# Kernel tuning notes

Hardware: AMD Instinct MI355X
Metric: run time of the kernel (lower is better)

Reference implementation:

```python
import jax, jax.numpy as jnp
import numpy as np

DEPTH = 6
INPUT_DIM = 512
HIDDEN = [128, 64]
OUT_DIM = 8
BATCH = 8192
NUM_LEAVES = 2 ** DEPTH            # 64
NUM_INTERNAL = 2 ** DEPTH - 1      # 63 routing Dense(1, sigmoid) nodes


def setup_inputs() -> dict:
    key = jax.random.key(0)
    ks = jax.random.split(key, 9)
    s = lambda fan_in: 1.0 / np.sqrt(fan_in)
    return {
        "x": jax.random.normal(ks[0], (BATCH, INPUT_DIM), dtype=jnp.float32),
        # routers: one Dense(input_dim -> 1) per internal node
        "router_W": jax.random.normal(ks[1], (NUM_INTERNAL, INPUT_DIM), dtype=jnp.float32) * s(INPUT_DIM),
        "router_b": jnp.zeros((NUM_INTERNAL,), dtype=jnp.float32),
        # leaf MLPs: Dense(512->128, relu) -> Dense(128->64, relu) -> Dense(64->8, linear), one per leaf
        "W1": jax.random.normal(ks[2], (NUM_LEAVES, INPUT_DIM, HIDDEN[0]), dtype=jnp.float32) * s(INPUT_DIM),
        "b1": jnp.zeros((NUM_LEAVES, HIDDEN[0]), dtype=jnp.float32),
        "W2": jax.random.normal(ks[3], (NUM_LEAVES, HIDDEN[0], HIDDEN[1]), dtype=jnp.float32) * s(HIDDEN[0]),
        "b2": jnp.zeros((NUM_LEAVES, HIDDEN[1]), dtype=jnp.float32),
        "W3": jax.random.normal(ks[4], (NUM_LEAVES, HIDDEN[1], OUT_DIM), dtype=jnp.float32) * s(HIDDEN[1]),
        "b3": jnp.zeros((NUM_LEAVES, OUT_DIM), dtype=jnp.float32),
    }


def reference(x, router_W, router_b, W1, b1, W2, b2, W3, b3):
    B = x.shape[0]
    depth = int(np.log2(router_W.shape[0] + 1))
    # All routing probabilities in one fused GEMM: [B, num_internal]
    route = jax.nn.sigmoid(jnp.einsum('bi,ni->bn', x, router_W) + router_b)
    # Soft routing down the tree: interleave left/right child probabilities per level.
    p = jnp.ones((B, 1), dtype=x.dtype)
    offset = 0
    for level in range(depth):  # small fixed loop over tree levels
        n = 2 ** level
        d = route[:, offset:offset + n]              # P(go left) at each node in level
        p = jnp.stack([p * d, p * (1.0 - d)], axis=-1).reshape(B, 2 * n)
        offset += n
    # p: [B, num_leaves] leaf arrival probabilities (sums to 1 per row)
    # Leaf experts as batched (grouped) GEMMs over the leaf axis l.
    h = jax.nn.relu(jnp.einsum('bi,lih->blh', x, W1) + b1)   # [B, L, 128]
    h = jax.nn.relu(jnp.einsum('blh,lhk->blk', h, W2) + b2)  # [B, L, 64]
    pred = jnp.einsum('blk,lko->blo', h, W3) + b3            # [B, L, out] (linear output act)
    # Weighted mixture over leaves.
    return jnp.einsum('bl,blo->bo', p, pred)                 # [B, out]
```

## Files before the change

kernel.cpp:

```cpp
#include <hip/hip_runtime.h>
#include <hip/hip_bf16.h>


typedef _Float16 f16;
typedef _Float16 f16x8 __attribute__((ext_vector_type(8)));
typedef float    f32x4 __attribute__((ext_vector_type(4)));
typedef float    f32x16 __attribute__((ext_vector_type(16)));

#define MFMA16(a,b,c) __builtin_amdgcn_mfma_f32_16x16x32_f16((a),(b),(c),0,0,0)
#define MFMA32(a,b,c) __builtin_amdgcn_mfma_f32_32x32x16_f16((a),(b),(c),0,0,0)

typedef const __attribute__((address_space(1))) void gv_t;
typedef __attribute__((address_space(3))) void lv_t;
__device__ __forceinline__ void cp16(const void* g, char* lds_dst) {
  __builtin_amdgcn_global_load_lds((gv_t*)g, (lv_t*)lds_dst, 16, 0, 0);
}

#define WS_XH    0u
#define WS_W1F   8388608u
#define WS_W2F   16777216u
#define WS_W3F   17825792u
#define WS_RWF   17956864u
#define WS_NEED  18022400u

#define L_X   0
#define L_H1  32768
#define L_H2  41472
#define L_P   46080
#define L_TOT 50176

__global__ __launch_bounds__(256) void prep_all(
    const float* __restrict__ x, const float* __restrict__ rW,
    const float* __restrict__ W1, const float* __restrict__ W2,
    const float* __restrict__ W3,
    f16* __restrict__ xh, f16* __restrict__ w1f, f16* __restrict__ w2f,
    f16* __restrict__ w3f, f16* __restrict__ rwf, float* __restrict__ out) {
  const int bid = blockIdx.x, t = threadIdx.x;
  if (bid < 512) {
    const int l = bid >> 3, kc = bid & 7;
    const int lane = t & 63;
#pragma unroll
    for (int p = 0; p < 4; ++p) {
      int c = p * 4 + (t >> 6);
      int ng = c >> 2, ksl = c & 3;
      int n = ng * 32 + (lane & 31);
      int k0 = kc * 64 + ksl * 16 + (lane >> 5) * 8;
      const float* src = W1 + ((size_t)l * 512 + k0) * 128 + n;
      f16x8 h;
#pragma unroll
      for (int j = 0; j < 8; ++j) h[j] = (f16)src[(size_t)j * 128];
      *(f16x8*)(w1f + ((size_t)((l * 4 + ng) * 32 + kc * 4 + ksl) * 64 + lane) * 8) = h;
    }
  } else if (bid < 768) {
    size_t base = (size_t)(bid - 512) * 16384;
#pragma unroll
    for (int i = 0; i < 8; ++i) {
      size_t idx = base + ((size_t)t + i * 256) * 8;
      float4 a = *(const float4*)(x + idx);
      float4 b = *(const float4*)(x + idx + 4);
      f16x8 h = {(f16)a.x,(f16)a.y,(f16)a.z,(f16)a.w,(f16)b.x,(f16)b.y,(f16)b.z,(f16)b.w};
      *(f16x8*)(xh + idx) = h;
    }
  } else if (bid < 832) {
    const int l = bid - 768;
    const int lane = t & 63;
#pragma unroll
    for (int p = 0; p < 4; ++p) {
      int c = p * 4 + (t >> 6);
      int nb = c >> 2, ks = c & 3;
      int n = nb * 16 + (lane & 15);
      int k0 = ks * 32 + (lane >> 4) * 8;
      const float* src = W2 + (size_t)l * 8192 + (size_t)k0 * 64 + n;
      f16x8 h;
#pragma unroll
      for (int j = 0; j < 8; ++j) h[j] = (f16)src[(size_t)j * 64];
      *(f16x8*)(w2f + ((size_t)((l * 4 + nb) * 4 + ks) * 64 + lane) * 8) = h;
    }
    if (t < 128) {
      int ks = t >> 6, lane2 = t & 63;
      int n = lane2 & 15;
      int k0 = ks * 32 + (lane2 >> 4) * 8;
      f16x8 h;
#pragma unroll
      for (int j = 0; j < 8; ++j)
        h[j] = (n < 8) ? (f16)W3[((size_t)l * 64 + k0 + j) * 8 + n] : (f16)0.f;
      *(f16x8*)(w3f + ((size_t)(l * 2 + ks) * 64 + lane2) * 8) = h;
    }
  } else {
    int c = (bid - 832) * 4 + (t >> 6);
    int ngr = c >> 5, ks = c & 31;
    int lane = t & 63;
    int n = ngr * 32 + (lane & 31);
    int k0 = ks * 16 + (lane >> 5) * 8;
    f16x8 h;
#pragma unroll
    for (int j = 0; j < 8; ++j)
      h[j] = (n < 63) ? (f16)rW[(size_t)n * 512 + k0 + j] : (f16)0.f;
    *(f16x8*)(rwf + ((size_t)c * 64 + lane) * 8) = h;
    size_t o0 = ((size_t)(bid - 832) * 256 + t) * 16;
    float4 z = {0.f, 0.f, 0.f, 0.f};
#pragma unroll
    for (int i = 0; i < 4; ++i) *(float4*)(out + o0 + i * 4) = z;
  }
}

__global__ __launch_bounds__(256, 2) void fused_tree(
    const f16* __restrict__ xh, const f16* __restrict__ w1f,
    const f16* __restrict__ w2f, const f16* __restrict__ w3f,
    const f16* __restrict__ rwf, const float* __restrict__ rb,
    const float* __restrict__ b1, const float* __restrict__ b2,
    const float* __restrict__ b3, float* __restrict__ out) {
  __shared__ char smem[L_TOT];
  f16*   x_lds   = (f16*)(smem + L_X);
  f16*   h1_lds  = (f16*)(smem + L_H1);
  float* route_s = (float*)(smem + L_H1);
  f16*   h2_lds  = (f16*)(smem + L_H2);
  float* p_lds   = (float*)(smem + L_P);

  const int t = threadIdx.x;
  const int w = t >> 6, L = t & 63;
  const int l16 = L & 15, quad = L >> 4;
  const int r31 = L & 31, kp = L >> 5;

  const int bid = blockIdx.x;
  const int r8 = bid & 7;
  const int lg0 = (r8 >> 1) * 16;
  const int btp = (bid >> 3) * 2 + (r8 & 1);
  const int b0 = btp * 64;

#pragma unroll
  for (int j = 0; j < 8; ++j) {
    int r = w * 8 + j;
    int u = (L & 56) | ((L & 7) ^ (r & 7));
    cp16(xh + (size_t)(b0 + 32 + r) * 512 + u * 8, smem + r * 1024);
  }
  f16x8 a0[32];
#pragma unroll
  for (int ks = 0; ks < 32; ++ks)
    a0[ks] = *(const f16x8*)(xh + (size_t)(b0 + r31) * 512 + ks * 16 + kp * 8);
  __syncthreads();

  {
    const int btr = w >> 1, ngr = w & 1;
    f32x16 accr;
#pragma unroll
    for (int i = 0; i < 16; ++i) accr[i] = 0.f;
    const f16* rbase = rwf + (size_t)(ngr * 32) * 512 + (size_t)L * 8;
#pragma unroll
    for (int ks = 0; ks < 32; ++ks) {
      f16x8 B = *(const f16x8*)(rbase + (size_t)ks * 512);
      f16x8 A;
      if (btr == 0) A = a0[ks];
      else {
        int u = ks * 2 + kp;
        A = *(const f16x8*)(x_lds + r31 * 512 + ((u & 56) | ((u & 7) ^ (r31 & 7))) * 8);
      }
      accr = MFMA32(A, B, accr);
    }
    int node = ngr * 32 + r31;
    float rbv = (node < 63) ? rb[node] : 0.f;
#pragma unroll
    for (int reg = 0; reg < 16; ++reg) {
      int rr = btr * 32 + (reg & 3) + 8 * (reg >> 2) + 4 * kp;
      route_s[rr * 68 + node] = 1.f / (1.f + __expf(-(accr[reg] + rbv)));
    }
  }
  __syncthreads();
  float prod[4];
  {
    int row = t >> 2, j0 = t & 3;
#pragma unroll
    for (int i = 0; i < 4; ++i) {
      int l = lg0 + j0 * 4 + i;
      float pr = 1.f;
#pragma unroll
      for (int lev = 0; lev < 6; ++lev) {
        int node = (1 << lev) - 1 + (l >> (6 - lev));
        float d = route_s[row * 68 + node];
        pr *= ((l >> (5 - lev)) & 1) ? (1.f - d) : d;
      }
      prod[i] = pr;
    }
  }
  __syncthreads();
  {
    int row = t >> 2, j0 = t & 3;
#pragma unroll
    for (int i = 0; i < 4; ++i) p_lds[row * 16 + j0 * 4 + i] = prod[i];
  }
  __syncthreads();

  const f16* w1base = w1f + ((size_t)(lg0 * 4 + w) * 32) * 512 + (size_t)L * 8;
  f16x8 bq[2][4];
#pragma unroll
  for (int s = 0; s < 4; ++s) bq[0][s] = *(const f16x8*)(w1base + (size_t)s * 512);

  f32x4 acc_out = {0.f, 0.f, 0.f, 0.f};
  const int mt = w >> 1, nt2 = w & 1;

#pragma unroll 1
  for (int li = 0; li < 16; ++li) {
    const int l = lg0 + li;
    const size_t leafoff = (size_t)li * 65536;

    f32x16 acc1r, acc1l;
#pragma unroll
    for (int i = 0; i < 16; ++i) { acc1r[i] = 0.f; acc1l[i] = 0.f; }

#pragma unroll
    for (int q = 0; q < 8; ++q) {
      f16x8 A1[4];
#pragma unroll
      for (int s = 0; s < 4; ++s) {
        int u = (q * 4 + s) * 2 + kp;
        A1[s] = *(const f16x8*)(x_lds + r31 * 512 + ((u & 56) | ((u & 7) ^ (r31 & 7))) * 8);
      }
      size_t nxt = (q < 7) ? (leafoff + (size_t)(q + 1) * 2048)
                           : ((li < 15) ? (leafoff + 65536) : (leafoff + 7 * 2048));
#pragma unroll
      for (int s = 0; s < 4; ++s)
        bq[(q + 1) & 1][s] = *(const f16x8*)(w1base + nxt + (size_t)s * 512);
      __builtin_amdgcn_s_setprio(1);
#pragma unroll
      for (int s = 0; s < 4; ++s)
        acc1r = MFMA32(a0[q * 4 + s], bq[q & 1][s], acc1r);
#pragma unroll
      for (int s = 0; s < 4; ++s)
        acc1l = MFMA32(A1[s], bq[q & 1][s], acc1l);
      __builtin_amdgcn_s_setprio(0);
    }

    f16x8 bw2[2][4];
#pragma unroll
    for (int n16 = 0; n16 < 2; ++n16)
#pragma unroll
      for (int ks = 0; ks < 4; ++ks)
        bw2[n16][ks] = *(const f16x8*)(w2f + ((size_t)((l * 4 + nt2 * 2 + n16) * 4 + ks) * 64 + L) * 8);
    f16x8 bw3[2];
#pragma unroll
    for (int ks = 0; ks < 2; ++ks)
      bw3[ks] = *(const f16x8*)(w3f + ((size_t)(l * 2 + ks) * 64 + L) * 8);

    const int n1 = w * 32 + r31;
    const float bias1 = b1[l * 128 + n1];

#pragma unroll
    for (int reg = 0; reg < 16; ++reg) {
      int rr = (reg & 3) + 8 * (reg >> 2) + 4 * kp;
      float v = acc1r[reg] + bias1;
      h1_lds[rr * 136 + n1] = (f16)(v > 0.f ? v : 0.f);
    }
    __syncthreads();

#define GEMM2_BT(btv)                                                          \
    {                                                                          \
      f32x4 acc2[2] = {{0.f,0.f,0.f,0.f},{0.f,0.f,0.f,0.f}};                   \
      _Pragma("unroll")                                                        \
      for (int ks = 0; ks < 4; ++ks) {                                         \
        f16x8 A = *(const f16x8*)(h1_lds + (mt * 16 + l16) * 136 + ks * 32 + quad * 8); \
        _Pragma("unroll")                                                      \
        for (int n16 = 0; n16 < 2; ++n16) acc2[n16] = MFMA16(A, bw2[n16][ks], acc2[n16]); \
      }                                                                        \
      _Pragma("unroll")                                                        \
      for (int n16 = 0; n16 < 2; ++n16) {                                      \
        int n2 = nt2 * 32 + n16 * 16 + l16;                                    \
        float bias2 = b2[l * 64 + n2];                                         \
        _Pragma("unroll")                                                      \
        for (int rg = 0; rg < 4; ++rg) {                                       \
          int r2 = mt * 16 + quad * 4 + rg;                                    \
          float v = acc2[n16][rg] + bias2;                                     \
          v = v > 0.f ? v : 0.f;                                               \
          h2_lds[r2 * 72 + n2] = (f16)(v * p_lds[((btv) * 32 + r2) * 16 + li]); \
        }                                                                      \
      }                                                                        \
    }

    GEMM2_BT(0)
    __syncthreads();

    if (w < 2) {
#pragma unroll
      for (int ks = 0; ks < 2; ++ks) {
        f16x8 A = *(const f16x8*)(h2_lds + ((w & 1) * 16 + l16) * 72 + ks * 32 + quad * 8);
        acc_out = MFMA16(A, bw3[ks], acc_out);
      }
    }
#pragma unroll
    for (int reg = 0; reg < 16; ++reg) {
      int rr = (reg & 3) + 8 * (reg >> 2) + 4 * kp;
      float v = acc1l[reg] + bias1;
      h1_lds[rr * 136 + n1] = (f16)(v > 0.f ? v : 0.f);
    }
    __syncthreads();

    GEMM2_BT(1)
    __syncthreads();

    if (w >= 2) {
#pragma unroll
      for (int ks = 0; ks < 2; ++ks) {
        f16x8 A = *(const f16x8*)(h2_lds + ((w & 1) * 16 + l16) * 72 + ks * 32 + quad * 8);
        acc_out = MFMA16(A, bw3[ks], acc_out);
      }
    }
#undef GEMM2_BT
  }

  if (l16 < 8) {
    const int btf = w >> 1, mtf = w & 1;
    float b3v[16];
#pragma unroll
    for (int li2 = 0; li2 < 16; ++li2) b3v[li2] = b3[(lg0 + li2) * 8 + l16];
#pragma unroll
    for (int rg = 0; rg < 4; ++rg) {
      int rloc = btf * 32 + mtf * 16 + quad * 4 + rg;
      float v = acc_out[rg];
#pragma unroll
      for (int li2 = 0; li2 < 16; ++li2) v += p_lds[rloc * 16 + li2] * b3v[li2];
      atomicAdd(out + (size_t)(b0 + rloc) * 8 + l16, v);
    }
  }
}

extern "C" void kernel_launch(void* const* d_in, const int* in_sizes, int n_in,
                              void* d_out, int out_size, void* d_ws, size_t ws_size,
                              hipStream_t stream) {
  const float* x  = (const float*)d_in[0];
  const float* rW = (const float*)d_in[1];
  const float* rb = (const float*)d_in[2];
  const float* W1 = (const float*)d_in[3];
  const float* b1 = (const float*)d_in[4];
  const float* W2 = (const float*)d_in[5];
  const float* b2 = (const float*)d_in[6];
  const float* W3 = (const float*)d_in[7];
  const float* b3 = (const float*)d_in[8];
  float* out = (float*)d_out;

  if (ws_size < WS_NEED) return;

  char* ws = (char*)d_ws;
  f16* xh  = (f16*)(ws + WS_XH);
  f16* w1f = (f16*)(ws + WS_W1F);
  f16* w2f = (f16*)(ws + WS_W2F);
  f16* w3f = (f16*)(ws + WS_W3F);
  f16* rwf = (f16*)(ws + WS_RWF);

  prep_all<<<848, 256, 0, stream>>>(x, rW, W1, W2, W3, xh, w1f, w2f, w3f, rwf, out);
  fused_tree<<<512, 256, 0, stream>>>(xh, w1f, w2f, w3f, rwf, rb, b1, b2, b3, out);
}
```

Measured before the change: 192.7 us.

## Merge prep and fused tree kernels into one cooperative launch with grid sync

Folds the fp16 conversion/prepack stage into the main fused kernel, with a cooperative grid-wide barrier between the prep phase and the compute phase. The 512 blocks each repack one W1 slice and optionally an x, W2/W3 or router chunk. The aim is to remove the second kernel launch and the gap between the two launches. A fallback to the original two-kernel path remains if occupancy or the cooperative launch fails. The cost is a grid-wide sync, an occupancy query on every call, and uneven prep work across blocks.

```diff
diff --git a/kernel.cpp b/kernel.cpp
--- a/kernel.cpp
+++ b/kernel.cpp
@@ -1,5 +1,8 @@
 #include <hip/hip_runtime.h>
 #include <hip/hip_bf16.h>
+#include <hip/hip_cooperative_groups.h>
+
+namespace cg = cooperative_groups;
 
 
 typedef _Float16 f16;
@@ -29,82 +32,86 @@
 #define L_P   46080
 #define L_TOT 50176
 
-__global__ __launch_bounds__(256) void prep_all(
-    const float* __restrict__ x, const float* __restrict__ rW,
-    const float* __restrict__ W1, const float* __restrict__ W2,
-    const float* __restrict__ W3,
-    f16* __restrict__ xh, f16* __restrict__ w1f, f16* __restrict__ w2f,
-    f16* __restrict__ w3f, f16* __restrict__ rwf, float* __restrict__ out) {
-  const int bid = blockIdx.x, t = threadIdx.x;
-  if (bid < 512) {
-    const int l = bid >> 3, kc = bid & 7;
-    const int lane = t & 63;
-#pragma unroll
-    for (int p = 0; p < 4; ++p) {
-      int c = p * 4 + (t >> 6);
-      int ng = c >> 2, ksl = c & 3;
-      int n = ng * 32 + (lane & 31);
-      int k0 = kc * 64 + ksl * 16 + (lane >> 5) * 8;
-      const float* src = W1 + ((size_t)l * 512 + k0) * 128 + n;
-      f16x8 h;
-#pragma unroll
-      for (int j = 0; j < 8; ++j) h[j] = (f16)src[(size_t)j * 128];
-      *(f16x8*)(w1f + ((size_t)((l * 4 + ng) * 32 + kc * 4 + ksl) * 64 + lane) * 8) = h;
-    }
-  } else if (bid < 768) {
-    size_t base = (size_t)(bid - 512) * 16384;
-#pragma unroll
-    for (int i = 0; i < 8; ++i) {
-      size_t idx = base + ((size_t)t + i * 256) * 8;
-      float4 a = *(const float4*)(x + idx);
-      float4 b = *(const float4*)(x + idx + 4);
-      f16x8 h = {(f16)a.x,(f16)a.y,(f16)a.z,(f16)a.w,(f16)b.x,(f16)b.y,(f16)b.z,(f16)b.w};
-      *(f16x8*)(xh + idx) = h;
-    }
-  } else if (bid < 832) {
-    const int l = bid - 768;
-    const int lane = t & 63;
-#pragma unroll
-    for (int p = 0; p < 4; ++p) {
-      int c = p * 4 + (t >> 6);
-      int nb = c >> 2, ks = c & 3;
-      int n = nb * 16 + (lane & 15);
-      int k0 = ks * 32 + (lane >> 4) * 8;
-      const float* src = W2 + (size_t)l * 8192 + (size_t)k0 * 64 + n;
-      f16x8 h;
-#pragma unroll
-      for (int j = 0; j < 8; ++j) h[j] = (f16)src[(size_t)j * 64];
-      *(f16x8*)(w2f + ((size_t)((l * 4 + nb) * 4 + ks) * 64 + lane) * 8) = h;
-    }
-    if (t < 128) {
-      int ks = t >> 6, lane2 = t & 63;
-      int n = lane2 & 15;
-      int k0 = ks * 32 + (lane2 >> 4) * 8;
-      f16x8 h;
-#pragma unroll
-      for (int j = 0; j < 8; ++j)
-        h[j] = (n < 8) ? (f16)W3[((size_t)l * 64 + k0 + j) * 8 + n] : (f16)0.f;
-      *(f16x8*)(w3f + ((size_t)(l * 2 + ks) * 64 + lane2) * 8) = h;
-    }
-  } else {
-    int c = (bid - 832) * 4 + (t >> 6);
-    int ngr = c >> 5, ks = c & 31;
-    int lane = t & 63;
-    int n = ngr * 32 + (lane & 31);
-    int k0 = ks * 16 + (lane >> 5) * 8;
+__device__ __forceinline__ void prep_w1_unit(int unit, const float* __restrict__ W1,
+                                             f16* __restrict__ w1f, int t) {
+  const int l = unit >> 3, kc = unit & 7;
+  const int lane = t & 63;
+#pragma unroll
+  for (int p = 0; p < 4; ++p) {
+    int c = p * 4 + (t >> 6);
+    int ng = c >> 2, ksl = c & 3;
+    int n = ng * 32 + (lane & 31);
+    int k0 = kc * 64 + ksl * 16 + (lane >> 5) * 8;
+    const float* src = W1 + ((size_t)l * 512 + k0) * 128 + n;
     f16x8 h;
 #pragma unroll
+    for (int j = 0; j < 8; ++j) h[j] = (f16)src[(size_t)j * 128];
+    *(f16x8*)(w1f + ((size_t)((l * 4 + ng) * 32 + kc * 4 + ksl) * 64 + lane) * 8) = h;
+  }
+}
+
+__device__ __forceinline__ void prep_xh_unit(int unit, const float* __restrict__ x,
+                                             f16* __restrict__ xh, int t) {
+  size_t base = (size_t)unit * 16384;
+#pragma unroll
+  for (int i = 0; i < 8; ++i) {
+    size_t idx = base + ((size_t)t + i * 256) * 8;
+    float4 a = *(const float4*)(x + idx);
+    float4 b = *(const float4*)(x + idx + 4);
+    f16x8 h = {(f16)a.x,(f16)a.y,(f16)a.z,(f16)a.w,(f16)b.x,(f16)b.y,(f16)b.z,(f16)b.w};
+    *(f16x8*)(xh + idx) = h;
+  }
+}
+
+__device__ __forceinline__ void prep_w23_unit(int l, const float* __restrict__ W2,
+                                              const float* __restrict__ W3,
+                                              f16* __restrict__ w2f,
+                                              f16* __restrict__ w3f, int t) {
+  const int lane = t & 63;
+#pragma unroll
+  for (int p = 0; p < 4; ++p) {
+    int c = p * 4 + (t >> 6);
+    int nb = c >> 2, ks = c & 3;
+    int n = nb * 16 + (lane & 15);
+    int k0 = ks * 32 + (lane >> 4) * 8;
+    const float* src = W2 + (size_t)l * 8192 + (size_t)k0 * 64 + n;
+    f16x8 h;
+#pragma unroll
+    for (int j = 0; j < 8; ++j) h[j] = (f16)src[(size_t)j * 64];
+    *(f16x8*)(w2f + ((size_t)((l * 4 + nb) * 4 + ks) * 64 + lane) * 8) = h;
+  }
+  if (t < 128) {
+    int ks = t >> 6, lane2 = t & 63;
+    int n = lane2 & 15;
+    int k0 = ks * 32 + (lane2 >> 4) * 8;
+    f16x8 h;
+#pragma unroll
     for (int j = 0; j < 8; ++j)
-      h[j] = (n < 63) ? (f16)rW[(size_t)n * 512 + k0 + j] : (f16)0.f;
-    *(f16x8*)(rwf + ((size_t)c * 64 + lane) * 8) = h;
-    size_t o0 = ((size_t)(bid - 832) * 256 + t) * 16;
-    float4 z = {0.f, 0.f, 0.f, 0.f};
-#pragma unroll
-    for (int i = 0; i < 4; ++i) *(float4*)(out + o0 + i * 4) = z;
-  }
-}
-
-__global__ __launch_bounds__(256, 2) void fused_tree(
+      h[j] = (n < 8) ? (f16)W3[((size_t)l * 64 + k0 + j) * 8 + n] : (f16)0.f;
+    *(f16x8*)(w3f + ((size_t)(l * 2 + ks) * 64 + lane2) * 8) = h;
+  }
+}
+
+__device__ __forceinline__ void prep_rwf_unit(int u, const float* __restrict__ rW,
+                                              f16* __restrict__ rwf,
+                                              float* __restrict__ out, int t) {
+  int c = u * 4 + (t >> 6);
+  int ngr = c >> 5, ks = c & 31;
+  int lane = t & 63;
+  int n = ngr * 32 + (lane & 31);
+  int k0 = ks * 16 + (lane >> 5) * 8;
+  f16x8 h;
+#pragma unroll
+  for (int j = 0; j < 8; ++j)
+    h[j] = (n < 63) ? (f16)rW[(size_t)n * 512 + k0 + j] : (f16)0.f;
+  *(f16x8*)(rwf + ((size_t)c * 64 + lane) * 8) = h;
+  size_t o0 = ((size_t)u * 256 + t) * 16;
+  float4 z = {0.f, 0.f, 0.f, 0.f};
+#pragma unroll
+  for (int i = 0; i < 4; ++i) *(float4*)(out + o0 + i * 4) = z;
+}
+
+__device__ __forceinline__ void fused_body(
     const f16* __restrict__ xh, const f16* __restrict__ w1f,
     const f16* __restrict__ w2f, const f16* __restrict__ w3f,
     const f16* __restrict__ rwf, const float* __restrict__ rb,
@@ -322,6 +329,46 @@
   }
 }
 
+__global__ __launch_bounds__(256, 2) void tree_all(
+    const float* __restrict__ x, const float* __restrict__ rW,
+    const float* __restrict__ W1, const float* __restrict__ W2,
+    const float* __restrict__ W3, const float* __restrict__ rb,
+    const float* __restrict__ b1, const float* __restrict__ b2,
+    const float* __restrict__ b3,
+    f16* __restrict__ xh, f16* __restrict__ w1f, f16* __restrict__ w2f,
+    f16* __restrict__ w3f, f16* __restrict__ rwf, float* __restrict__ out) {
+  const int bid = blockIdx.x, t = threadIdx.x;
+  prep_w1_unit(bid, W1, w1f, t);
+  if (bid < 256)      prep_xh_unit(bid, x, xh, t);
+  else if (bid < 320) prep_w23_unit(bid - 256, W2, W3, w2f, w3f, t);
+  else if (bid < 336) prep_rwf_unit(bid - 320, rW, rwf, out, t);
+  __threadfence();
+  cg::this_grid().sync();
+  fused_body(xh, w1f, w2f, w3f, rwf, rb, b1, b2, b3, out);
+}
+
+__global__ __launch_bounds__(256) void prep_all(
+    const float* __restrict__ x, const float* __restrict__ rW,
+    const float* __restrict__ W1, const float* __restrict__ W2,
+    const float* __restrict__ W3,
+    f16* __restrict__ xh, f16* __restrict__ w1f, f16* __restrict__ w2f,
+    f16* __restrict__ w3f, f16* __restrict__ rwf, float* __restrict__ out) {
+  const int bid = blockIdx.x, t = threadIdx.x;
+  if (bid < 512)      prep_w1_unit(bid, W1, w1f, t);
+  else if (bid < 768) prep_xh_unit(bid - 512, x, xh, t);
+  else if (bid < 832) prep_w23_unit(bid - 768, W2, W3, w2f, w3f, t);
+  else                prep_rwf_unit(bid - 832, rW, rwf, out, t);
+}
+
+__global__ __launch_bounds__(256, 2) void fused_tree(
+    const f16* __restrict__ xh, const f16* __restrict__ w1f,
+    const f16* __restrict__ w2f, const f16* __restrict__ w3f,
+    const f16* __restrict__ rwf, const float* __restrict__ rb,
+    const float* __restrict__ b1, const float* __restrict__ b2,
+    const float* __restrict__ b3, float* __restrict__ out) {
+  fused_body(xh, w1f, w2f, w3f, rwf, rb, b1, b2, b3, out);
+}
+
 extern "C" void kernel_launch(void* const* d_in, const int* in_sizes, int n_in,
                               void* d_out, int out_size, void* d_ws, size_t ws_size,
                               hipStream_t stream) {
@@ -345,6 +392,22 @@
   f16* w3f = (f16*)(ws + WS_W3F);
   f16* rwf = (f16*)(ws + WS_RWF);
 
-  prep_all<<<848, 256, 0, stream>>>(x, rW, W1, W2, W3, xh, w1f, w2f, w3f, rwf, out);
-  fused_tree<<<512, 256, 0, stream>>>(xh, w1f, w2f, w3f, rwf, rb, b1, b2, b3, out);
-}
+  int maxb = 0;
+  hipError_t oe = hipOccupancyMaxActiveBlocksPerMultiprocessor(
+      &maxb, reinterpret_cast<const void*>(tree_all), 256, 0);
+  bool coop_done = false;
+  if (oe == hipSuccess && maxb >= 2) {
+    void* kargs[] = {(void*)&x, (void*)&rW, (void*)&W1, (void*)&W2, (void*)&W3,
+                     (void*)&rb, (void*)&b1, (void*)&b2, (void*)&b3,
+                     (void*)&xh, (void*)&w1f, (void*)&w2f, (void*)&w3f,
+                     (void*)&rwf, (void*)&out};
+    hipError_t le = hipLaunchCooperativeKernel(
+        reinterpret_cast<const void*>(tree_all), dim3(512), dim3(256),
+        kargs, 0, stream);
+    coop_done = (le == hipSuccess);
+  }
+  if (!coop_done) {
+    prep_all<<<848, 256, 0, stream>>>(x, rW, W1, W2, W3, xh, w1f, w2f, w3f, rwf, out);
+    fused_tree<<<512, 256, 0, stream>>>(xh, w1f, w2f, w3f, rwf, rb, b1, b2, b3, out);
+  }
+}
```

Result: no change. 193.5 us (+0.4%).
